# Kernel optimization log

Hardware: AMD Instinct MI355X
Metric: run time of the kernel (lower is better)

The kernel has to match this reference:

```python
import jax, jax.numpy as jnp
import numpy as np

C = 256      # channels (multiple of 32 for GroupNorm)
K = 3        # kernel
PAD = 1      # padding
G = 32       # GroupNorm groups
EPS = 1e-5


def setup_inputs() -> dict:
    key = jax.random.key(0)
    ks = jax.random.split(key, 7)
    B, H, W = 4, 64, 64
    return {
        "x": jax.random.normal(ks[0], (B, C, H, W), jnp.float32),
        "offset": jax.random.normal(ks[1], (B, 2 * K * K, H, W), jnp.float32),
        "weight": jax.random.normal(ks[2], (C, C, K, K), jnp.float32) * 0.01,
        "att_w": jax.random.normal(ks[3], (1, C), jnp.float32) * 0.01,
        "att_b": jnp.zeros((1,), jnp.float32),
        "gamma": jnp.ones((C,), jnp.float32),
        "beta": jnp.zeros((C,), jnp.float32),
    }


def _bilinear_one(xb, py, px):
    # xb: [C, H, W]; py, px: [KK, H, W] fractional sample coords (zero-pad outside)
    H, W = xb.shape[1], xb.shape[2]
    y0 = jnp.floor(py)
    x0 = jnp.floor(px)
    y1 = y0 + 1.0
    x1 = x0 + 1.0
    wy1 = py - y0
    wy0 = 1.0 - wy1
    wx1 = px - x0
    wx0 = 1.0 - wx1

    def g(yi, xi):
        valid = (yi >= 0) & (yi < H) & (xi >= 0) & (xi < W)
        yc = jnp.clip(yi, 0, H - 1).astype(jnp.int32)
        xc = jnp.clip(xi, 0, W - 1).astype(jnp.int32)
        return xb[:, yc, xc] * valid[None].astype(xb.dtype)  # [C, KK, H, W]

    return (g(y0, x0) * (wy0 * wx0)[None] + g(y0, x1) * (wy0 * wx1)[None]
            + g(y1, x0) * (wy1 * wx0)[None] + g(y1, x1) * (wy1 * wx1)[None])


def reference(x, offset, weight, att_w, att_b, gamma, beta):
    B, Cc, H, W = x.shape
    KK = K * K
    off = offset.reshape(B, KK, 2, H, W)  # (dy, dx) per kernel tap
    ii, jj = jnp.meshgrid(jnp.arange(K), jnp.arange(K), indexing='ij')
    dky = (ii - PAD).reshape(KK).astype(x.dtype)
    dkx = (jj - PAD).reshape(KK).astype(x.dtype)
    ys = jnp.arange(H, dtype=x.dtype)
    xs = jnp.arange(W, dtype=x.dtype)
    # sample coords [B, KK, H, W]
    py = ys[None, :, None] + dky[:, None, None] + off[:, :, 0]
    px = xs[None, None, :] + dkx[:, None, None] + off[:, :, 1]

    # deformable unfold: [B, C, KK, H, W]
    xu = jax.vmap(_bilinear_one)(x, py, px)

    # max over kernel taps -> channel attention gate
    xm = xu.max(axis=2)  # [B, C, H, W]
    att = jax.nn.sigmoid(jnp.einsum('bchw,oc->bohw', xm, att_w)
                         + att_b[None, :, None, None])  # [B, 1, H, W]

    # gate the unfolded samples, then emulate the conv as one GEMM
    xw = xu * att[:, :, None]  # broadcast over C, KK
    cols = xw.transpose(1, 2, 0, 3, 4).reshape(Cc * KK, B * H * W)  # [C*KK, BHW]
    out = (weight.reshape(Cc, Cc * KK) @ cols).reshape(Cc, B, H, W).transpose(1, 0, 2, 3)

    # GroupNorm(32, C) + ReLU
    og = out.reshape(B, G, Cc // G, H, W)
    mu = og.mean(axis=(2, 3, 4), keepdims=True)
    var = og.var(axis=(2, 3, 4), keepdims=True)
    on = ((og - mu) * jax.lax.rsqrt(var + EPS)).reshape(B, Cc, H, W)
    return jax.nn.relu(on * gamma[None, :, None, None] + beta[None, :, None, None])
```

## Files before the change

kernel.cpp:

```cpp
#include <hip/hip_runtime.h>

#define CT 256
#define KDIM 2304
#define CSZ2 9216

typedef unsigned short u16;
typedef _Float16 h2 __attribute__((ext_vector_type(2)));
typedef _Float16 h8 __attribute__((ext_vector_type(8)));
typedef __attribute__((ext_vector_type(4))) float f32x4;

__device__ __forceinline__ unsigned pkh(float a, float b) {
    h2 r; r[0] = (_Float16)a; r[1] = (_Float16)b;
    return __builtin_bit_cast(unsigned, r);
}

__global__ __launch_bounds__(256) void k_prep(const float* __restrict__ x, uint4* __restrict__ xi,
                                              const float* __restrict__ wgt, uint4* __restrict__ pw)
{
    if (blockIdx.x < 2048) {
        int u = blockIdx.x * 256 + threadIdx.x;
        int bcg = u >> 12, p = u & 4095;
        const float* xp = x + (((size_t)bcg) << 15) + p;
        unsigned r[4];
#pragma unroll
        for (int i = 0; i < 4; ++i)
            r[i] = pkh(xp[(size_t)(2 * i) << 12], xp[(size_t)(2 * i + 1) << 12]);
        uint4 o; o.x = r[0]; o.y = r[1]; o.z = r[2]; o.w = r[3];
        xi[u] = o;
    } else {
        int u = (blockIdx.x - 2048) * 256 + threadIdx.x;
        int kc = u >> 10, rm = u & 1023;
        int m = rm >> 2, j = rm & 3;
        int round = kc / 9, tap = kc - round * 9;
        const float* src = wgt + (size_t)m * KDIM + tap;
        int c0 = round * 32 + j * 8;
        unsigned q[4];
#pragma unroll
        for (int i = 0; i < 4; ++i)
            q[i] = pkh(src[(size_t)(c0 + 2 * i) * 9], src[(size_t)(c0 + 2 * i + 1) * 9]);
        uint4 o; o.x = q[0]; o.y = q[1]; o.z = q[2]; o.w = q[3];
        pw[u] = o;
    }
}

struct GB {
    uint4 c00, c01, c10, c11;
    unsigned wx, wy;
    int dst;
};

__device__ __forceinline__ void g_load(int it, int round, size_t xib,
                                       const uint2* s_wt, const int2* s_off,
                                       const uint4* __restrict__ xi, GB& g)
{
    int sp = it / 288;
    int rem = it - sp * 288;
    uint2 wp = s_wt[rem];
    int2 of = s_off[rem];
    g.wx = wp.x; g.wy = wp.y;
    const uint4* gp = xi + xib + ((size_t)((round << 2) + sp) << 12);
    g.c00 = gp[of.x & 0xffff];
    g.c01 = gp[(unsigned)of.x >> 16];
    g.c10 = gp[of.y & 0xffff];
    g.c11 = gp[(unsigned)of.y >> 16];
    g.dst = it * 8;
}

__device__ __forceinline__ void g_fin(const GB& g, u16* colb)
{
    h2 w01 = __builtin_bit_cast(h2, g.wx);
    h2 w23 = __builtin_bit_cast(h2, g.wy);
    h2 wxp = (h2){w01[0], w01[0]}, wyp = (h2){w01[1], w01[1]};
    h2 wzp = (h2){w23[0], w23[0]}, wwp = (h2){w23[1], w23[1]};
    const unsigned* a00 = (const unsigned*)&g.c00;
    const unsigned* a01 = (const unsigned*)&g.c01;
    const unsigned* a10 = (const unsigned*)&g.c10;
    const unsigned* a11 = (const unsigned*)&g.c11;
    unsigned o[4];
#pragma unroll
    for (int q = 0; q < 4; ++q) {
        h2 rr = wxp * __builtin_bit_cast(h2, a00[q]) + wyp * __builtin_bit_cast(h2, a01[q])
              + wzp * __builtin_bit_cast(h2, a10[q]) + wwp * __builtin_bit_cast(h2, a11[q]);
        o[q] = __builtin_bit_cast(unsigned, rr);
    }
    uint4 ov; ov.x = o[0]; ov.y = o[1]; ov.z = o[2]; ov.w = o[3];
    *(uint4*)&colb[g.dst] = ov;
}

__global__ __launch_bounds__(512, 4) void k_main(const uint4* __restrict__ xi, const float* __restrict__ off,
                                                 const uint4* __restrict__ pw, const float* __restrict__ att_w,
                                                 const float* __restrict__ att_b,
                                                 float* __restrict__ outp, float* __restrict__ gnpart)
{
    __shared__ uint2 s_wt[288];
    __shared__ int2 s_off[288];
    __shared__ u16 col[2 * CSZ2];
    __shared__ float s_att[32];

    int bid = blockIdx.x;
    int xcd = bid & 7, idx = bid >> 3;
    int b = xcd >> 1;
    int local = ((xcd & 1) << 6) + idx;
    int h = local >> 1, half = local & 1;
    int lbid = b * 128 + local;
    int n0 = half * 32;

    int tid = threadIdx.x;
    int lane = tid & 63, w = tid >> 6;
    int l15 = lane & 15, kb = lane >> 4;
    int wm = w * 32;
    int nn_a = w * 4 + (lane >> 4);
    int ca = (lane & 15) * 2;

    for (int e = tid; e < 288; e += 512) {
        int kk = e >> 5, wl = e & 31;
        int ww_ = n0 + wl;
        int ky = kk / 3, kx = kk - ky * 3;
        float dy = off[((size_t)(b * 18 + 2 * kk) * 64 + h) * 64 + ww_];
        float dx = off[((size_t)(b * 18 + 2 * kk + 1) * 64 + h) * 64 + ww_];
        float py = (float)(h + ky - 1) + dy;
        float px = (float)(ww_ + kx - 1) + dx;
        float y0f = floorf(py), x0f = floorf(px);
        int y0 = (int)y0f, x0 = (int)x0f;
        float fy = py - y0f, fx = px - x0f;
        float vy0 = (y0 >= 0 && y0 < 64) ? 1.f : 0.f;
        float vy1 = (y0 >= -1 && y0 < 63) ? 1.f : 0.f;
        float vx0 = (x0 >= 0 && x0 < 64) ? 1.f : 0.f;
        float vx1 = (x0 >= -1 && x0 < 63) ? 1.f : 0.f;
        float w0 = (1.f - fy) * (1.f - fx) * vy0 * vx0;
        float w1 = (1.f - fy) * fx * vy0 * vx1;
        float w2 = fy * (1.f - fx) * vy1 * vx0;
        float w3 = fy * fx * vy1 * vx1;
        uint2 wp;
        wp.x = pkh(w0, w1);
        wp.y = pkh(w2, w3);
        int yc0 = min(max(y0, 0), 63), yc1 = min(max(y0 + 1, 0), 63);
        int xc0 = min(max(x0, 0), 63), xc1 = min(max(x0 + 1, 0), 63);
        s_wt[e] = wp;
        s_off[e] = make_int2((yc0 * 64 + xc0) | ((yc0 * 64 + xc1) << 16),
                             (yc1 * 64 + xc0) | ((yc1 * 64 + xc1) << 16));
    }

    size_t xib = (size_t)(b * 32) << 12;

    float att_acc = 0.f;
    f32x4 acc[2][2];
#pragma unroll
    for (int mt = 0; mt < 2; ++mt)
#pragma unroll
        for (int nt = 0; nt < 2; ++nt) acc[mt][nt] = (f32x4){0.f, 0.f, 0.f, 0.f};

    int pwoff[2];
#pragma unroll
    for (int mt = 0; mt < 2; ++mt) pwoff[mt] = (wm + mt * 16 + l15) * 4 + kb;

    __syncthreads();

    {
        GB g0, g1, g2;
        g_load(tid, 0, xib, s_wt, s_off, xi, g0);
        g_load(tid + 512, 0, xib, s_wt, s_off, xi, g1);
        g_fin(g0, col);
        if (tid < 128) g_load(tid + 1024, 0, xib, s_wt, s_off, xi, g2);
        g_fin(g1, col);
        if (tid < 128) g_fin(g2, col);
    }

    uint4 aa[3][2];
#pragma unroll
    for (int ts = 0; ts < 3; ++ts)
#pragma unroll
        for (int mt = 0; mt < 2; ++mt)
            aa[ts][mt] = pw[(size_t)ts * 1024 + pwoff[mt]];

    __syncthreads();

    for (int r = 0; r < 8; ++r) {
        u16* cb = col + (r & 1) * CSZ2;
        u16* nb = col + ((r & 1) ^ 1) * CSZ2;

        GB g0, g1, g2;
        if (r < 7) g_load(tid, r + 1, xib, s_wt, s_off, xi, g0);

        {
            int spa = ca >> 3, co = ca & 7;
            const u16* base = &cb[spa * 2304 + nn_a * 8 + co];
            float m0 = -1e30f, m1 = -1e30f;
#pragma unroll
            for (int t = 0; t < 9; ++t) {
                unsigned v = *(const unsigned*)(base + t * 256);
                h2 vv = __builtin_bit_cast(h2, v);
                m0 = fmaxf(m0, (float)vv[0]);
                m1 = fmaxf(m1, (float)vv[1]);
            }
            int cbx = r * 32 + ca;
            att_acc += att_w[cbx] * m0 + att_w[cbx + 1] * m1;
        }

#pragma unroll
        for (int ts = 0; ts < 9; ++ts) {
            h8 bf[2];
#pragma unroll
            for (int nt = 0; nt < 2; ++nt)
                bf[nt] = *(const h8*)&cb[kb * 2304 + ts * 256 + (nt * 16 + l15) * 8];
            h8 af[2];
#pragma unroll
            for (int mt = 0; mt < 2; ++mt) af[mt] = __builtin_bit_cast(h8, aa[ts % 3][mt]);
            if (ts + 3 < 9) {
#pragma unroll
                for (int mt = 0; mt < 2; ++mt)
                    aa[ts % 3][mt] = pw[(size_t)(r * 9 + ts + 3) * 1024 + pwoff[mt]];
            } else if (r < 7) {
#pragma unroll
                for (int mt = 0; mt < 2; ++mt)
                    aa[ts % 3][mt] = pw[(size_t)((r + 1) * 9 + (ts - 6)) * 1024 + pwoff[mt]];
            }
#pragma unroll
            for (int mt = 0; mt < 2; ++mt)
#pragma unroll
                for (int nt = 0; nt < 2; ++nt)
                    acc[mt][nt] = __builtin_amdgcn_mfma_f32_16x16x32_f16(af[mt], bf[nt], acc[mt][nt], 0, 0, 0);
            if (ts == 1 && r < 7) {
                g_fin(g0, nb);
                g_load(tid + 512, r + 1, xib, s_wt, s_off, xi, g1);
            }
            if (ts == 5 && r < 7) {
                g_fin(g1, nb);
                if (tid < 128) g_load(tid + 1024, r + 1, xib, s_wt, s_off, xi, g2);
            }
        }
        if (r < 7 && tid < 128) g_fin(g2, nb);
        __syncthreads();
    }

#pragma unroll
    for (int d = 1; d <= 8; d <<= 1) att_acc += __shfl_xor(att_acc, d);
    if ((lane & 15) == 0) s_att[nn_a] = 1.f / (1.f + expf(-(att_acc + att_b[0])));
    __syncthreads();

    float attn[2];
#pragma unroll
    for (int nt = 0; nt < 2; ++nt) attn[nt] = s_att[nt * 16 + l15];

#pragma unroll
    for (int mt = 0; mt < 2; ++mt) {
        float s1 = 0.f, s2 = 0.f;
#pragma unroll
        for (int nt = 0; nt < 2; ++nt)
#pragma unroll
            for (int r = 0; r < 4; ++r) {
                float v = acc[mt][nt][r] * attn[nt];
                int m = wm + mt * 16 + kb * 4 + r;
                outp[(((size_t)(b * CT + m)) << 12) + h * 64 + n0 + nt * 16 + l15] = v;
                s1 += v; s2 += v * v;
            }
#pragma unroll
        for (int d = 1; d <= 16; d <<= 1) {
            s1 += __shfl_xor(s1, d);
            s2 += __shfl_xor(s2, d);
        }
        if ((lane & 31) == 0) {
            int gidx = w * 4 + mt * 2 + (kb >> 1);
            gnpart[lbid * 64 + gidx * 2] = s1;
            gnpart[lbid * 64 + gidx * 2 + 1] = s2;
        }
    }
}

__global__ __launch_bounds__(256) void k_gn(const float* __restrict__ gnpart, const float* __restrict__ gamma,
                                            const float* __restrict__ beta, float* __restrict__ outp)
{
    __shared__ float rs1[128], rs2[128];
    __shared__ float s_stat[2];
    int bg = blockIdx.x;
    int b = bg >> 5, g = bg & 31;
    int tid = threadIdx.x;
    if (tid < 128) {
        int blk = (b * 64 + (tid >> 1)) * 2 + (tid & 1);
        rs1[tid] = gnpart[blk * 64 + g * 2];
        rs2[tid] = gnpart[blk * 64 + g * 2 + 1];
    }
    __syncthreads();
    if (tid < 64) {
        float a = rs1[tid] + rs1[tid + 64];
        float c = rs2[tid] + rs2[tid + 64];
#pragma unroll
        for (int d = 1; d <= 32; d <<= 1) {
            a += __shfl_xor(a, d);
            c += __shfl_xor(c, d);
        }
        if (tid == 0) {
            float mean = a * (1.f / 32768.f);
            float var = c * (1.f / 32768.f) - mean * mean;
            s_stat[0] = mean;
            s_stat[1] = rsqrtf(var + 1e-5f);
        }
    }
    __syncthreads();
    float mean = s_stat[0], rstd = s_stat[1];
    float4* p4 = (float4*)(outp + ((size_t)(b * CT + g * 8) << 12));
    for (int i = tid; i < 8192; i += 256) {
        int c = g * 8 + (i >> 10);
        float ga = gamma[c], be = beta[c];
        float4 v = p4[i];
        float4 r;
        r.x = fmaxf((v.x - mean) * rstd * ga + be, 0.f);
        r.y = fmaxf((v.y - mean) * rstd * ga + be, 0.f);
        r.z = fmaxf((v.z - mean) * rstd * ga + be, 0.f);
        r.w = fmaxf((v.w - mean) * rstd * ga + be, 0.f);
        p4[i] = r;
    }
}

extern "C" void kernel_launch(void* const* d_in, const int* in_sizes, int n_in,
                              void* d_out, int out_size, void* d_ws, size_t ws_size,
                              hipStream_t stream)
{
    const float* x = (const float*)d_in[0];
    const float* off = (const float*)d_in[1];
    const float* wgt = (const float*)d_in[2];
    const float* attw = (const float*)d_in[3];
    const float* attb = (const float*)d_in[4];
    const float* gamma = (const float*)d_in[5];
    const float* beta = (const float*)d_in[6];
    float* outp = (float*)d_out;

    char* ws = (char*)d_ws;
    uint4* xi = (uint4*)ws;
    uint4* pw = (uint4*)(ws + 8388608);
    float* gnpart = (float*)(ws + 9568256);

    k_prep<<<dim3(2336), dim3(256), 0, stream>>>(x, xi, wgt, pw);
    k_main<<<dim3(512), dim3(512), 0, stream>>>(xi, off, pw, attw, attb, outp, gnpart);
    k_gn<<<dim3(128), dim3(256), 0, stream>>>(gnpart, gamma, beta, outp);
}
```

Before: 163.8 us.

## Split k_main into dedicated gather producer waves and MFMA consumer waves

Adds two extra waves per block that only perform the bilinear gather into the double-buffered col tile, while the original eight waves only do the attention max and MFMA GEMM. The col tile layout gets an XOR swizzle on the pixel index to reduce LDS bank conflicts on reads. This is meant to decouple gather latency from the matrix core loop. The catch is that gather throughput now rests on 128 threads per block and the block grows to 640 threads, which raises register pressure.

```diff
diff --git a/kernel.cpp b/kernel.cpp
--- a/kernel.cpp
+++ b/kernel.cpp
@@ -46,7 +46,6 @@
 struct GB {
     uint4 c00, c01, c10, c11;
     unsigned wx, wy;
-    int dst;
 };
 
 __device__ __forceinline__ void g_load(int it, int round, size_t xib,
@@ -63,10 +62,9 @@
     g.c01 = gp[(unsigned)of.x >> 16];
     g.c10 = gp[of.y & 0xffff];
     g.c11 = gp[(unsigned)of.y >> 16];
-    g.dst = it * 8;
-}
-
-__device__ __forceinline__ void g_fin(const GB& g, u16* colb)
+}
+
+__device__ __forceinline__ void g_fin(const GB& g, int it, u16* colb)
 {
     h2 w01 = __builtin_bit_cast(h2, g.wx);
     h2 w23 = __builtin_bit_cast(h2, g.wy);
@@ -83,18 +81,36 @@
               + wzp * __builtin_bit_cast(h2, a10[q]) + wwp * __builtin_bit_cast(h2, a11[q]);
         o[q] = __builtin_bit_cast(unsigned, rr);
     }
+    int sp = it / 288;
+    int rem = it - sp * 288;
+    int dst = (sp * 288 + (rem >> 5) * 32 + ((rem & 31) ^ sp)) * 8;
     uint4 ov; ov.x = o[0]; ov.y = o[1]; ov.z = o[2]; ov.w = o[3];
-    *(uint4*)&colb[g.dst] = ov;
-}
-
-__global__ __launch_bounds__(512, 4) void k_main(const uint4* __restrict__ xi, const float* __restrict__ off,
+    *(uint4*)&colb[dst] = ov;
+}
+
+__device__ __forceinline__ void gather_round(int p, int rnd, size_t xib,
+                                             const uint2* s_wt, const int2* s_off,
+                                             const uint4* __restrict__ xi, u16* dstbuf)
+{
+    GB ga, gb;
+    g_load(p, rnd, xib, s_wt, s_off, xi, ga);
+#pragma unroll
+    for (int j = 0; j < 9; j += 2) {
+        if (j + 1 < 9) g_load((j + 1) * 128 + p, rnd, xib, s_wt, s_off, xi, gb);
+        g_fin(ga, j * 128 + p, dstbuf);
+        if (j + 2 < 9) g_load((j + 2) * 128 + p, rnd, xib, s_wt, s_off, xi, ga);
+        if (j + 1 < 9) g_fin(gb, (j + 1) * 128 + p, dstbuf);
+    }
+}
+
+__global__ __launch_bounds__(640, 5) void k_main(const uint4* __restrict__ xi, const float* __restrict__ off,
                                                  const uint4* __restrict__ pw, const float* __restrict__ att_w,
                                                  const float* __restrict__ att_b,
                                                  float* __restrict__ outp, float* __restrict__ gnpart)
 {
     __shared__ uint2 s_wt[288];
     __shared__ int2 s_off[288];
-    __shared__ u16 col[2 * CSZ2];
+    __shared__ __align__(16) u16 col[2 * CSZ2];
     __shared__ float s_att[32];
 
     int bid = blockIdx.x;
@@ -107,12 +123,8 @@
 
     int tid = threadIdx.x;
     int lane = tid & 63, w = tid >> 6;
-    int l15 = lane & 15, kb = lane >> 4;
-    int wm = w * 32;
-    int nn_a = w * 4 + (lane >> 4);
-    int ca = (lane & 15) * 2;
-
-    for (int e = tid; e < 288; e += 512) {
+
+    for (int e = tid; e < 288; e += 640) {
         int kk = e >> 5, wl = e & 31;
         int ww_ = n0 + wl;
         int ky = kk / 3, kx = kk - ky * 3;
@@ -143,127 +155,123 @@
 
     size_t xib = (size_t)(b * 32) << 12;
 
-    float att_acc = 0.f;
-    f32x4 acc[2][2];
-#pragma unroll
-    for (int mt = 0; mt < 2; ++mt)
-#pragma unroll
-        for (int nt = 0; nt < 2; ++nt) acc[mt][nt] = (f32x4){0.f, 0.f, 0.f, 0.f};
-
-    int pwoff[2];
-#pragma unroll
-    for (int mt = 0; mt < 2; ++mt) pwoff[mt] = (wm + mt * 16 + l15) * 4 + kb;
-
     __syncthreads();
 
-    {
-        GB g0, g1, g2;
-        g_load(tid, 0, xib, s_wt, s_off, xi, g0);
-        g_load(tid + 512, 0, xib, s_wt, s_off, xi, g1);
-        g_fin(g0, col);
-        if (tid < 128) g_load(tid + 1024, 0, xib, s_wt, s_off, xi, g2);
-        g_fin(g1, col);
-        if (tid < 128) g_fin(g2, col);
-    }
-
-    uint4 aa[3][2];
-#pragma unroll
-    for (int ts = 0; ts < 3; ++ts)
+    if (w < 8) {
+        int l15 = lane & 15, kb = lane >> 4;
+        int wm = w * 32;
+        int nn_a = w * 4 + (lane >> 4);
+        int ca = (lane & 15) * 2;
+
+        float att_acc = 0.f;
+        f32x4 acc[2][2];
 #pragma unroll
         for (int mt = 0; mt < 2; ++mt)
-            aa[ts][mt] = pw[(size_t)ts * 1024 + pwoff[mt]];
-
-    __syncthreads();
-
-    for (int r = 0; r < 8; ++r) {
-        u16* cb = col + (r & 1) * CSZ2;
-        u16* nb = col + ((r & 1) ^ 1) * CSZ2;
-
-        GB g0, g1, g2;
-        if (r < 7) g_load(tid, r + 1, xib, s_wt, s_off, xi, g0);
-
-        {
-            int spa = ca >> 3, co = ca & 7;
-            const u16* base = &cb[spa * 2304 + nn_a * 8 + co];
-            float m0 = -1e30f, m1 = -1e30f;
-#pragma unroll
-            for (int t = 0; t < 9; ++t) {
-                unsigned v = *(const unsigned*)(base + t * 256);
-                h2 vv = __builtin_bit_cast(h2, v);
-                m0 = fmaxf(m0, (float)vv[0]);
-                m1 = fmaxf(m1, (float)vv[1]);
+#pragma unroll
+            for (int nt = 0; nt < 2; ++nt) acc[mt][nt] = (f32x4){0.f, 0.f, 0.f, 0.f};
+
+        int pwoff[2];
+#pragma unroll
+        for (int mt = 0; mt < 2; ++mt) pwoff[mt] = (wm + mt * 16 + l15) * 4 + kb;
+
+        uint4 aa[3][2];
+#pragma unroll
+        for (int ts = 0; ts < 3; ++ts)
+#pragma unroll
+            for (int mt = 0; mt < 2; ++mt)
+                aa[ts][mt] = pw[(size_t)ts * 1024 + pwoff[mt]];
+
+        __syncthreads();
+
+        for (int r = 0; r < 8; ++r) {
+            const u16* cb = col + (r & 1) * CSZ2;
+
+            {
+                int spa = ca >> 3, co = ca & 7;
+                const u16* base = &cb[spa * 2304 + ((nn_a ^ spa)) * 8 + co];
+                float m0 = -1e30f, m1 = -1e30f;
+#pragma unroll
+                for (int t = 0; t < 9; ++t) {
+                    unsigned v = *(const unsigned*)(base + t * 256);
+                    h2 vv = __builtin_bit_cast(h2, v);
+                    m0 = fmaxf(m0, (float)vv[0]);
+                    m1 = fmaxf(m1, (float)vv[1]);
+                }
+                int cbx = r * 32 + ca;
+                att_acc += att_w[cbx] * m0 + att_w[cbx + 1] * m1;
             }
-            int cbx = r * 32 + ca;
-            att_acc += att_w[cbx] * m0 + att_w[cbx + 1] * m1;
-        }
-
-#pragma unroll
-        for (int ts = 0; ts < 9; ++ts) {
-            h8 bf[2];
+
+#pragma unroll
+            for (int ts = 0; ts < 9; ++ts) {
+                h8 bf[2];
+#pragma unroll
+                for (int nt = 0; nt < 2; ++nt)
+                    bf[nt] = *(const h8*)&cb[kb * 2304 + ts * 256 + (((nt * 16 + l15) ^ kb)) * 8];
+                h8 af[2];
+#pragma unroll
+                for (int mt = 0; mt < 2; ++mt) af[mt] = __builtin_bit_cast(h8, aa[ts % 3][mt]);
+                if (ts + 3 < 9) {
+#pragma unroll
+                    for (int mt = 0; mt < 2; ++mt)
+                        aa[ts % 3][mt] = pw[(size_t)(r * 9 + ts + 3) * 1024 + pwoff[mt]];
+                } else if (r < 7) {
+#pragma unroll
+                    for (int mt = 0; mt < 2; ++mt)
+                        aa[ts % 3][mt] = pw[(size_t)((r + 1) * 9 + (ts - 6)) * 1024 + pwoff[mt]];
+                }
+#pragma unroll
+                for (int mt = 0; mt < 2; ++mt)
+#pragma unroll
+                    for (int nt = 0; nt < 2; ++nt)
+                        acc[mt][nt] = __builtin_amdgcn_mfma_f32_16x16x32_f16(af[mt], bf[nt], acc[mt][nt], 0, 0, 0);
+            }
+            __syncthreads();
+        }
+
+#pragma unroll
+        for (int d = 1; d <= 8; d <<= 1) att_acc += __shfl_xor(att_acc, d);
+        if ((lane & 15) == 0) s_att[nn_a] = 1.f / (1.f + expf(-(att_acc + att_b[0])));
+        __syncthreads();
+
+        float attn[2];
+#pragma unroll
+        for (int nt = 0; nt < 2; ++nt) attn[nt] = s_att[nt * 16 + l15];
+
+#pragma unroll
+        for (int mt = 0; mt < 2; ++mt) {
+            float s1 = 0.f, s2 = 0.f;
 #pragma unroll
             for (int nt = 0; nt < 2; ++nt)
-                bf[nt] = *(const h8*)&cb[kb * 2304 + ts * 256 + (nt * 16 + l15) * 8];
-            h8 af[2];
-#pragma unroll
-            for (int mt = 0; mt < 2; ++mt) af[mt] = __builtin_bit_cast(h8, aa[ts % 3][mt]);
-            if (ts + 3 < 9) {
-#pragma unroll
-                for (int mt = 0; mt < 2; ++mt)
-                    aa[ts % 3][mt] = pw[(size_t)(r * 9 + ts + 3) * 1024 + pwoff[mt]];
-            } else if (r < 7) {
-#pragma unroll
-                for (int mt = 0; mt < 2; ++mt)
-                    aa[ts % 3][mt] = pw[(size_t)((r + 1) * 9 + (ts - 6)) * 1024 + pwoff[mt]];
+#pragma unroll
+                for (int r = 0; r < 4; ++r) {
+                    float v = acc[mt][nt][r] * attn[nt];
+                    int m = wm + mt * 16 + kb * 4 + r;
+                    outp[(((size_t)(b * CT + m)) << 12) + h * 64 + n0 + nt * 16 + l15] = v;
+                    s1 += v; s2 += v * v;
+                }
+#pragma unroll
+            for (int d = 1; d <= 16; d <<= 1) {
+                s1 += __shfl_xor(s1, d);
+                s2 += __shfl_xor(s2, d);
             }
-#pragma unroll
-            for (int mt = 0; mt < 2; ++mt)
-#pragma unroll
-                for (int nt = 0; nt < 2; ++nt)
-                    acc[mt][nt] = __builtin_amdgcn_mfma_f32_16x16x32_f16(af[mt], bf[nt], acc[mt][nt], 0, 0, 0);
-            if (ts == 1 && r < 7) {
-                g_fin(g0, nb);
-                g_load(tid + 512, r + 1, xib, s_wt, s_off, xi, g1);
+            if ((lane & 31) == 0) {
+                int gidx = w * 4 + mt * 2 + (kb >> 1);
+                gnpart[lbid * 64 + gidx * 2] = s1;
+                gnpart[lbid * 64 + gidx * 2 + 1] = s2;
             }
-            if (ts == 5 && r < 7) {
-                g_fin(g1, nb);
-                if (tid < 128) g_load(tid + 1024, r + 1, xib, s_wt, s_off, xi, g2);
-            }
-        }
-        if (r < 7 && tid < 128) g_fin(g2, nb);
+        }
+    } else {
+        int p = tid - 512;
+
+        gather_round(p, 0, xib, s_wt, s_off, xi, col);
         __syncthreads();
-    }
-
-#pragma unroll
-    for (int d = 1; d <= 8; d <<= 1) att_acc += __shfl_xor(att_acc, d);
-    if ((lane & 15) == 0) s_att[nn_a] = 1.f / (1.f + expf(-(att_acc + att_b[0])));
-    __syncthreads();
-
-    float attn[2];
-#pragma unroll
-    for (int nt = 0; nt < 2; ++nt) attn[nt] = s_att[nt * 16 + l15];
-
-#pragma unroll
-    for (int mt = 0; mt < 2; ++mt) {
-        float s1 = 0.f, s2 = 0.f;
-#pragma unroll
-        for (int nt = 0; nt < 2; ++nt)
-#pragma unroll
-            for (int r = 0; r < 4; ++r) {
-                float v = acc[mt][nt][r] * attn[nt];
-                int m = wm + mt * 16 + kb * 4 + r;
-                outp[(((size_t)(b * CT + m)) << 12) + h * 64 + n0 + nt * 16 + l15] = v;
-                s1 += v; s2 += v * v;
-            }
-#pragma unroll
-        for (int d = 1; d <= 16; d <<= 1) {
-            s1 += __shfl_xor(s1, d);
-            s2 += __shfl_xor(s2, d);
-        }
-        if ((lane & 31) == 0) {
-            int gidx = w * 4 + mt * 2 + (kb >> 1);
-            gnpart[lbid * 64 + gidx * 2] = s1;
-            gnpart[lbid * 64 + gidx * 2 + 1] = s2;
-        }
+
+        for (int r = 0; r < 8; ++r) {
+            if (r < 7)
+                gather_round(p, r + 1, xib, s_wt, s_off, xi, col + ((r + 1) & 1) * CSZ2);
+            __syncthreads();
+        }
+        __syncthreads();
     }
 }
 
@@ -331,6 +339,6 @@
     float* gnpart = (float*)(ws + 9568256);
 
     k_prep<<<dim3(2336), dim3(256), 0, stream>>>(x, xi, wgt, pw);
-    k_main<<<dim3(512), dim3(512), 0, stream>>>(xi, off, pw, attw, attb, outp, gnpart);
+    k_main<<<dim3(512), dim3(640), 0, stream>>>(xi, off, pw, attw, attb, outp, gnpart);
     k_gn<<<dim3(128), dim3(256), 0, stream>>>(gnpart, gamma, beta, outp);
 }
```

Result: slower. 177.7 us (+8.5%).
